# Kernel tuning notes

Measured on AMD Instinct MI355X. Metric: run time of the kernel, lower is better.

The kernel has to match this reference:

```python
import jax, jax.numpy as jnp
import numpy as np

ALPHA = 0.85  # position gain (init kwarg alpha)
BETA = 0.005  # velocity gain (init kwarg beta)


def setup_inputs() -> dict:
    key = jax.random.key(0)
    Z = jax.random.normal(key, (4096, 8192), dtype=jnp.float32)
    return {"Z": Z}


def reference(Z) -> jnp.ndarray:
    # alpha-beta (g-h) filter recurrence, scanned over the time axis.
    #   diff = z - p;  x = p + a*diff;  v += b*diff;  p = x + v
    # Initial state: p = Z[:, 0], v = 0  (so x_0 == Z[:, 0]).
    a = jnp.asarray(ALPHA, Z.dtype)
    b = jnp.asarray(BETA, Z.dtype)

    def step(carry, z):
        p, v = carry
        diff = z - p
        x = p + a * diff
        v = v + b * diff
        p = x + v
        return (p, v), x

    p0 = Z[:, 0]
    v0 = jnp.zeros_like(p0)
    # scan over time: Z.T has shape [T, B]
    _, xs = jax.lax.scan(step, (p0, v0), Z.T)
    return xs.T  # [B, T]
```

## Files before the change

kernel.cpp:

```cpp
#include <hip/hip_runtime.h>


#define A_CONST 0.85f
#define B_CONST 0.005f

constexpr int ROWS  = 4096;
constexpr int T     = 8192;
constexpr int W     = 2048;
constexpr int L     = 32;
constexpr int NSEC  = T / W;
constexpr int STRIDE = 33;

__global__ __launch_bounds__(256)
void kalman_kernel(const float* __restrict__ Z, float* __restrict__ X) {
    const int wave = threadIdx.x >> 6;
    const int lane = threadIdx.x & 63;
    const int row  = blockIdx.x * 4 + wave;

    __shared__ float lds[4][64 * STRIDE];
    float* buf = lds[wave];

    const float* Zr = Z + (size_t)row * T;
    float*       Xr = X + (size_t)row * T;

    double a00 = 1.0 - (double)A_CONST - (double)B_CONST, a01 = 1.0;
    double a10 = -(double)B_CONST,                        a11 = 1.0;
    #pragma unroll
    for (int i = 0; i < 5; ++i) {
        double n00 = a00*a00 + a01*a10;
        double n01 = a00*a01 + a01*a11;
        double n10 = a10*a00 + a11*a10;
        double n11 = a10*a01 + a11*a11;
        a00 = n00; a01 = n01; a10 = n10; a11 = n11;
    }
    const float A32_00 = (float)a00, A32_01 = (float)a01;
    const float A32_10 = (float)a10, A32_11 = (float)a11;

    float ps = Zr[0];
    float vs = 0.0f;

    for (int sec = 0; sec < NSEC; ++sec) {
        const float4* src = (const float4*)(Zr + sec * W);
        #pragma unroll
        for (int i = 0; i < W / 4 / 64; ++i) {
            int f = i * 64 + lane;
            float4 v4 = src[f];
            int c = f >> 3;
            int j = (f & 7) << 2;
            float* p = buf + c * STRIDE + j;
            p[0] = v4.x; p[1] = v4.y; p[2] = v4.z; p[3] = v4.w;
        }
        __syncthreads();

        float bp, bv;
        {
            float p = 0.0f, v = 0.0f;
            const float* zc = buf + lane * STRIDE;
            #pragma unroll
            for (int j = 0; j < L; ++j) {
                float z    = zc[j];
                float diff = z - p;
                float x    = p + A_CONST * diff;
                v += B_CONST * diff;
                p  = x + v;
            }
            bp = p; bv = v;
        }

        float sA00 = A32_00, sA01 = A32_01, sA10 = A32_10, sA11 = A32_11;
        float sb0 = bp, sb1 = bv;
        #pragma unroll
        for (int d = 1; d < 64; d <<= 1) {
            float oA00 = __shfl_up(sA00, d);
            float oA01 = __shfl_up(sA01, d);
            float oA10 = __shfl_up(sA10, d);
            float oA11 = __shfl_up(sA11, d);
            float ob0  = __shfl_up(sb0,  d);
            float ob1  = __shfl_up(sb1,  d);
            if (lane >= d) {
                float n00 = sA00*oA00 + sA01*oA10;
                float n01 = sA00*oA01 + sA01*oA11;
                float n10 = sA10*oA00 + sA11*oA10;
                float n11 = sA10*oA01 + sA11*oA11;
                float nb0 = sA00*ob0 + sA01*ob1 + sb0;
                float nb1 = sA10*ob0 + sA11*ob1 + sb1;
                sA00 = n00; sA01 = n01; sA10 = n10; sA11 = n11;
                sb0 = nb0; sb1 = nb1;
            }
        }

        float eA00 = __shfl_up(sA00, 1);
        float eA01 = __shfl_up(sA01, 1);
        float eA10 = __shfl_up(sA10, 1);
        float eA11 = __shfl_up(sA11, 1);
        float eb0  = __shfl_up(sb0,  1);
        float eb1  = __shfl_up(sb1,  1);
        if (lane == 0) { eA00 = 1.f; eA01 = 0.f; eA10 = 0.f; eA11 = 1.f; eb0 = 0.f; eb1 = 0.f; }

        float iA00 = __shfl(sA00, 63);
        float iA01 = __shfl(sA01, 63);
        float iA10 = __shfl(sA10, 63);
        float iA11 = __shfl(sA11, 63);
        float ib0  = __shfl(sb0,  63);
        float ib1  = __shfl(sb1,  63);

        {
            float p = eA00*ps + eA01*vs + eb0;
            float v = eA10*ps + eA11*vs + eb1;
            float* zc = buf + lane * STRIDE;
            #pragma unroll
            for (int j = 0; j < L; ++j) {
                float z    = zc[j];
                float diff = z - p;
                float x    = p + A_CONST * diff;
                v += B_CONST * diff;
                p  = x + v;
                zc[j] = x;
            }
        }

        {
            float np = iA00*ps + iA01*vs + ib0;
            float nv = iA10*ps + iA11*vs + ib1;
            ps = np; vs = nv;
        }

        __syncthreads();

        float4* dst = (float4*)(Xr + sec * W);
        #pragma unroll
        for (int i = 0; i < W / 4 / 64; ++i) {
            int f = i * 64 + lane;
            int c = f >> 3;
            int j = (f & 7) << 2;
            const float* p = buf + c * STRIDE + j;
            dst[f] = make_float4(p[0], p[1], p[2], p[3]);
        }
        __syncthreads();
    }
}

extern "C" void kernel_launch(void* const* d_in, const int* in_sizes, int n_in,
                              void* d_out, int out_size, void* d_ws, size_t ws_size,
                              hipStream_t stream) {
    const float* Z = (const float*)d_in[0];
    float*       X = (float*)d_out;
    dim3 grid(ROWS / 4), block(256);
    hipLaunchKernelGGL(kalman_kernel, grid, block, 0, stream, Z, X);
}
```

Baseline: 47.03 us.

## Prefetch next section into registers, one wave per block, nontemporal stores

Each block now holds a single 64-lane wave handling one row, so the block-wide barriers only synchronise one wave. The next section's Z values are loaded into registers while the current section is being processed, which overlaps global load latency with the scan. The section's inputs are also kept in a register array so the second pass does not re-read LDS, and output stores use nontemporal hints. The cost is more registers per thread (prefetch buffer plus a 32-float cache), which may reduce occupancy.

```diff
diff --git a/kernel.cpp b/kernel.cpp
--- a/kernel.cpp
+++ b/kernel.cpp
@@ -4,21 +4,21 @@
 #define A_CONST 0.85f
 #define B_CONST 0.005f
 
-constexpr int ROWS  = 4096;
-constexpr int T     = 8192;
-constexpr int W     = 2048;
-constexpr int L     = 32;
-constexpr int NSEC  = T / W;
+typedef float vfloat4 __attribute__((ext_vector_type(4)));
+
+constexpr int ROWS   = 4096;
+constexpr int T      = 8192;
+constexpr int W      = 2048;
+constexpr int L      = 32;
+constexpr int NSEC   = T / W;
 constexpr int STRIDE = 33;
 
-__global__ __launch_bounds__(256)
+__global__ __launch_bounds__(64)
 void kalman_kernel(const float* __restrict__ Z, float* __restrict__ X) {
-    const int wave = threadIdx.x >> 6;
-    const int lane = threadIdx.x & 63;
-    const int row  = blockIdx.x * 4 + wave;
+    const int lane = threadIdx.x;
+    const int row  = blockIdx.x;
 
-    __shared__ float lds[4][64 * STRIDE];
-    float* buf = lds[wave];
+    __shared__ float buf[64 * STRIDE];
 
     const float* Zr = Z + (size_t)row * T;
     float*       Xr = X + (size_t)row * T;
@@ -39,19 +39,32 @@
     float ps = Zr[0];
     float vs = 0.0f;
 
+    float4 r[8];
+    {
+        const float4* src = (const float4*)Zr;
+        #pragma unroll
+        for (int i = 0; i < 8; ++i) r[i] = src[i * 64 + lane];
+    }
+
     for (int sec = 0; sec < NSEC; ++sec) {
-        const float4* src = (const float4*)(Zr + sec * W);
         #pragma unroll
-        for (int i = 0; i < W / 4 / 64; ++i) {
+        for (int i = 0; i < 8; ++i) {
             int f = i * 64 + lane;
-            float4 v4 = src[f];
             int c = f >> 3;
             int j = (f & 7) << 2;
             float* p = buf + c * STRIDE + j;
-            p[0] = v4.x; p[1] = v4.y; p[2] = v4.z; p[3] = v4.w;
+            p[0] = r[i].x; p[1] = r[i].y; p[2] = r[i].z; p[3] = r[i].w;
         }
+
+        if (sec + 1 < NSEC) {
+            const float4* src = (const float4*)(Zr + (sec + 1) * W);
+            #pragma unroll
+            for (int i = 0; i < 8; ++i) r[i] = src[i * 64 + lane];
+        }
+
         __syncthreads();
 
+        float c32[L];
         float bp, bv;
         {
             float p = 0.0f, v = 0.0f;
@@ -59,6 +72,7 @@
             #pragma unroll
             for (int j = 0; j < L; ++j) {
                 float z    = zc[j];
+                c32[j]     = z;
                 float diff = z - p;
                 float x    = p + A_CONST * diff;
                 v += B_CONST * diff;
@@ -110,7 +124,7 @@
             float* zc = buf + lane * STRIDE;
             #pragma unroll
             for (int j = 0; j < L; ++j) {
-                float z    = zc[j];
+                float z    = c32[j];
                 float diff = z - p;
                 float x    = p + A_CONST * diff;
                 v += B_CONST * diff;
@@ -127,15 +141,19 @@
 
         __syncthreads();
 
-        float4* dst = (float4*)(Xr + sec * W);
-        #pragma unroll
-        for (int i = 0; i < W / 4 / 64; ++i) {
-            int f = i * 64 + lane;
-            int c = f >> 3;
-            int j = (f & 7) << 2;
-            const float* p = buf + c * STRIDE + j;
-            dst[f] = make_float4(p[0], p[1], p[2], p[3]);
+        {
+            vfloat4* dst = (vfloat4*)(Xr + sec * W);
+            #pragma unroll
+            for (int i = 0; i < 8; ++i) {
+                int f = i * 64 + lane;
+                int c = f >> 3;
+                int j = (f & 7) << 2;
+                const float* p = buf + c * STRIDE + j;
+                vfloat4 v4 = { p[0], p[1], p[2], p[3] };
+                __builtin_nontemporal_store(v4, dst + f);
+            }
         }
+
         __syncthreads();
     }
 }
@@ -145,6 +163,6 @@
                               hipStream_t stream) {
     const float* Z = (const float*)d_in[0];
     float*       X = (float*)d_out;
-    dim3 grid(ROWS / 4), block(256);
+    dim3 grid(ROWS), block(64);
     hipLaunchKernelGGL(kalman_kernel, grid, block, 0, stream, Z, X);
 }
```

After: 45.58 us. -3.1%, faster.
